# Kernel tuning notes

Measured on AMD Instinct MI355X. Metric: run time of the kernel, lower is better.

## Reference

```python
import jax, jax.numpy as jnp
import numpy as np

B, S, E, H = 2, 2048, 1024, 16
DH = E // H


def setup_inputs() -> dict:
    key = jax.random.key(0)
    ks = jax.random.split(key, 12)
    std = 1.0 / np.sqrt(E)
    inp = {
        "query": jax.random.normal(ks[0], (B, S, E), jnp.float32),
        "key": jax.random.normal(ks[1], (B, S, E), jnp.float32),
        "value": jax.random.normal(ks[2], (B, S, E), jnp.float32),
        "mask": jax.random.randint(ks[3], (B, 1, 1, S), 0, 2, jnp.int32),
        "Wq": jax.random.normal(ks[4], (E, E), jnp.float32) * std,
        "bq": jnp.zeros((E,), jnp.float32),
        "Wk": jax.random.normal(ks[5], (E, E), jnp.float32) * std,
        "bk": jnp.zeros((E,), jnp.float32),
        "Wv": jax.random.normal(ks[6], (E, E), jnp.float32) * std,
        "bv": jnp.zeros((E,), jnp.float32),
        "Wo": jax.random.normal(ks[7], (E, E), jnp.float32) * std,
        "bo": jnp.zeros((E,), jnp.float32),
    }
    return inp


def reference(query, key, value, mask, Wq, bq, Wk, bk, Wv, bv, Wo, bo):
    b = query.shape[0]
    # QKV projections, then split heads: [B,S,E] -> [B,H,S,Dh]
    def split_heads(x):
        return x.reshape(b, -1, H, DH).transpose(0, 2, 1, 3)
    q = split_heads(query @ Wq + bq)
    k = split_heads(key @ Wk + bk)
    v = split_heads(value @ Wv + bv)
    # explicit bmm -> mask -> softmax -> bmm (non-SDPA), scores [B,H,Sq,Sk]
    scores = jnp.einsum("bhqd,bhkd->bhqk", q, k) / np.sqrt(DH).astype(np.float32)
    scores = jnp.where(mask == 0, jnp.float32(-1e9), scores)
    attn = jax.nn.softmax(scores, axis=-1)  # dropout is identity in eval mode
    out = jnp.einsum("bhqk,bhkd->bhqd", attn, v)
    out = out.transpose(0, 2, 1, 3).reshape(b, -1, E)  # merge heads
    return out @ Wo + bo
```

## Files before the change

kernel.cpp:

```cpp
#include <hip/hip_runtime.h>
#include <hip/hip_bf16.h>
#include <stdint.h>

#define B_ 2
#define S_ 2048
#define E_ 1024
#define H_ 16
#define DH_ 64
#define MELEMS (4096 * 1024)
#define WE (1024 * 1024)

typedef unsigned short u16;
typedef __bf16 bf16x8 __attribute__((ext_vector_type(8)));
typedef u16 u16x8 __attribute__((ext_vector_type(8)));
typedef u16 u16x4 __attribute__((ext_vector_type(4)));
typedef float f32x4 __attribute__((ext_vector_type(4)));
typedef uint32_t u32x4 __attribute__((ext_vector_type(4)));
typedef uint32_t u32x2v __attribute__((ext_vector_type(2)));

__device__ __forceinline__ float bf2f(u16 u) {
    union { uint32_t i; float f; } v; v.i = ((uint32_t)u) << 16; return v.f;
}
__device__ __forceinline__ u16 f2bf(float f) {
    union { float f; uint32_t i; } v; v.f = f;
    uint32_t r = (v.i + 0x7FFFu + ((v.i >> 16) & 1u)) >> 16;
    return (u16)r;
}
__device__ __forceinline__ uint32_t pkbf(float a, float b) {
    __hip_bfloat162 h = __float22bfloat162_rn(make_float2(a, b));
    uint32_t r; __builtin_memcpy(&r, &h, 4);
    return r;
}
__device__ __forceinline__ bf16x8 ldfrag(const u16* p) {
    u16x8 t = *(const u16x8*)p;
    return __builtin_bit_cast(bf16x8, t);
}
__device__ __forceinline__ void gld16(const void* g, void* l) {
    __builtin_amdgcn_global_load_lds(
        (const __attribute__((address_space(1))) void*)g,
        (__attribute__((address_space(3))) void*)l, 16, 0, 0);
}

__global__ __launch_bounds__(256)
void cvt_all(const float* __restrict__ q, const float* __restrict__ k,
             const float* __restrict__ v,
             const float* __restrict__ W0, const float* __restrict__ W1,
             const float* __restrict__ W2, const float* __restrict__ W3,
             u16* __restrict__ Qi, u16* __restrict__ Ki, u16* __restrict__ Vi,
             u16* __restrict__ T0, u16* __restrict__ T1,
             u16* __restrict__ T2, u16* __restrict__ T3)
{
    __shared__ float tile[64][65];
    const int bid = blockIdx.x;
    const int tid = threadIdx.x;

    if (bid < 6144) {
        const int z = bid >> 11;
        const int cx = bid & 2047;
        const float* src = (z == 0) ? q : (z == 1) ? k : v;
        u16* dst = (z == 0) ? Qi : (z == 1) ? Ki : Vi;
        const size_t i8 = ((size_t)cx * 256 + tid) * 8;
        float4 f0 = *(const float4*)&src[i8];
        float4 f1 = *(const float4*)&src[i8 + 4];
        u16x8 t;
        t[0] = f2bf(f0.x); t[1] = f2bf(f0.y); t[2] = f2bf(f0.z); t[3] = f2bf(f0.w);
        t[4] = f2bf(f1.x); t[5] = f2bf(f1.y); t[6] = f2bf(f1.z); t[7] = f2bf(f1.w);
        *(u16x8*)&dst[i8] = t;
    } else {
        const int rr = bid - 6144;
        const int z = rr >> 8;
        const int tt = rr & 255;
        const float* W = (z == 0) ? W0 : (z == 1) ? W1 : (z == 2) ? W2 : W3;
        u16* T = (z == 0) ? T0 : (z == 1) ? T1 : (z == 2) ? T2 : T3;
        const int n0 = (tt & 15) * 64, k0 = (tt >> 4) * 64;
        const int r = tid >> 2, c0 = (tid & 3) * 16;

        #pragma unroll
        for (int i = 0; i < 4; ++i) {
            float4 w = *(const float4*)&W[(size_t)(k0 + r) * 1024 + n0 + c0 + i * 4];
            tile[r][c0 + i * 4 + 0] = w.x; tile[r][c0 + i * 4 + 1] = w.y;
            tile[r][c0 + i * 4 + 2] = w.z; tile[r][c0 + i * 4 + 3] = w.w;
        }
        __syncthreads();
        u16x8 a, b;
        #pragma unroll
        for (int j = 0; j < 8; ++j) a[j] = f2bf(tile[c0 + j][r]);
        #pragma unroll
        for (int j = 0; j < 8; ++j) b[j] = f2bf(tile[c0 + 8 + j][r]);
        *(u16x8*)&T[(size_t)(n0 + r) * 1024 + k0 + c0] = a;
        *(u16x8*)&T[(size_t)(n0 + r) * 1024 + k0 + c0 + 8] = b;
    }
}

template<int BN>
__global__ __launch_bounds__(256)
void gemm_bt(const u16* __restrict__ A0, const u16* __restrict__ A1,
             const u16* __restrict__ A2,
             const u16* __restrict__ Bt0, const u16* __restrict__ Bt1,
             const u16* __restrict__ Bt2,
             const float* __restrict__ b0, const float* __restrict__ b1,
             const float* __restrict__ b2,
             void* __restrict__ C0, void* __restrict__ C1, void* __restrict__ C2,
             const int* __restrict__ mask,
             int c_f32, int vt_z, float scale0, int K)
{
    const int z = blockIdx.z;
    const u16* A  = (z == 0) ? A0 : (z == 1) ? A1 : A2;
    const u16* Bt = (z == 0) ? Bt0 : (z == 1) ? Bt1 : Bt2;
    const float* bias = (z == 0) ? b0 : (z == 1) ? b1 : b2;
    void* C = (z == 0) ? C0 : (z == 1) ? C1 : C2;
    const float scale = (z == 0) ? scale0 : 1.0f;

    __shared__ alignas(16) u16 As[128 * 32];
    __shared__ alignas(16) u16 Bs[BN * 32];

    const int tid  = threadIdx.x;
    const int lane = tid & 63;
    const int wv   = tid >> 6;
    const int l15  = lane & 15;
    const int quad = lane >> 4;
    const int m0 = blockIdx.y * 128;
    const int n0 = blockIdx.x * BN;
    const int wr = (wv >> 1) * 64;
    const int wc = (wv & 1) * (BN / 2);

    const int srow = wv * 16 + (lane >> 2);
    const int skk  = (lane & 3) * 8;

    constexpr int NJ = BN / 32;
    f32x4 acc[4][NJ] = {};

    for (int k0 = 0; k0 < K; k0 += 32) {
        __syncthreads();
        #pragma unroll
        for (int h = 0; h < 2; ++h) {
            const int r = h * 64 + srow;
            gld16(&A[(size_t)(m0 + r) * K + k0 + skk], &As[r * 32 + skk]);
        }
        #pragma unroll
        for (int h = 0; h < BN / 64; ++h) {
            const int r = h * 64 + srow;
            gld16(&Bt[(size_t)(n0 + r) * K + k0 + skk], &Bs[r * 32 + skk]);
        }
        __syncthreads();

        bf16x8 a[4], b[NJ];
        #pragma unroll
        for (int i = 0; i < 4; ++i)
            a[i] = ldfrag(&As[(wr + i * 16 + l15) * 32 + quad * 8]);
        #pragma unroll
        for (int j = 0; j < NJ; ++j)
            b[j] = ldfrag(&Bs[(wc + j * 16 + l15) * 32 + quad * 8]);
        #pragma unroll
        for (int i = 0; i < 4; ++i)
            #pragma unroll
            for (int j = 0; j < NJ; ++j)
                acc[i][j] = __builtin_amdgcn_mfma_f32_16x16x32_bf16(
                    a[i], b[j], acc[i][j], 0, 0, 0);
    }

    #pragma unroll
    for (int j = 0; j < NJ; ++j) {
        const int col = n0 + wc + j * 16 + l15;
        const float bcol = bias[col];
        #pragma unroll
        for (int i = 0; i < 4; ++i) {
            if (z == vt_z) {
                const int row0 = m0 + wr + i * 16 + quad * 4;
                const int bb = row0 >> 11, s0 = row0 & 2047;
                const int4 mv = *(const int4*)&mask[bb * S_ + s0];
                u16x4 t;
                t[0] = mv.x ? f2bf((acc[i][j][0] + bcol) * scale) : (u16)0;
                t[1] = mv.y ? f2bf((acc[i][j][1] + bcol) * scale) : (u16)0;
                t[2] = mv.z ? f2bf((acc[i][j][2] + bcol) * scale) : (u16)0;
                t[3] = mv.w ? f2bf((acc[i][j][3] + bcol) * scale) : (u16)0;
                *(u16x4*)&((u16*)C)[((size_t)bb * E_ + col) * S_ + s0] = t;
            } else {
                #pragma unroll
                for (int r = 0; r < 4; ++r) {
                    const int row = m0 + wr + i * 16 + quad * 4 + r;
                    const float v = (acc[i][j][r] + bcol) * scale;
                    if (c_f32) ((float*)C)[(size_t)row * 1024 + col] = v;
                    else       ((u16*)C)[(size_t)row * 1024 + col]  = f2bf(v);
                }
            }
        }
    }
}

__global__ __launch_bounds__(512, 4)
void attn_v7(const u16* __restrict__ Q, const u16* __restrict__ K,
             const u16* __restrict__ Vt_g, const int* __restrict__ mask,
             u16* __restrict__ ctx)
{
    __shared__ alignas(16) u16 Ks[2][64 * 64];
    __shared__ alignas(16) u16 Vs[2][64 * 64];
    __shared__ alignas(16) u16 Mbf[S_];

    const int tid  = threadIdx.x;
    const int lane = tid & 63;
    const int wv   = tid >> 6;
    const int l15  = lane & 15;
    const int quad = lane >> 4;
    const int sw   = l15 & 7;
    const int kq   = (quad & 1) * 2 + (quad >> 1);
    const int qt = blockIdx.x;
    const int bh = blockIdx.y;
    const int b  = bh >> 4, h = bh & 15;

    const size_t qk_off = (size_t)b * S_ * E_ + (size_t)h * DH_;
    const size_t vt_off = ((size_t)b * E_ + (size_t)h * DH_) * S_;
    const int* mrow = &mask[b * S_];

    {
        const int i = tid * 4;
        const int4 m = *(const int4*)&mrow[i];
        u16x4 t;
        t[0] = m.x ? (u16)0x3F80 : (u16)0;
        t[1] = m.y ? (u16)0x3F80 : (u16)0;
        t[2] = m.z ? (u16)0x3F80 : (u16)0;
        t[3] = m.w ? (u16)0x3F80 : (u16)0;
        *(u16x4*)&Mbf[i] = t;
    }

    const int qr = qt * 128 + wv * 16 + l15;
    const bf16x8 qa0 = ldfrag(&Q[qk_off + (size_t)qr * E_ + quad * 8]);
    const bf16x8 qa1 = ldfrag(&Q[qk_off + (size_t)qr * E_ + 32 + quad * 8]);

    f32x4 oacc[4] = {};
    f32x4 lacc = {};

    const int kidx = tid & 255;
    const int grp  = tid >> 8;
    const int srow = kidx >> 3;
    const int sp   = kidx & 7;
    const int sg   = sp ^ (srow & 7);

    auto stage = [&](int kc, int buf) {
        #pragma unroll
        for (int g = 0; g < 2; ++g) {
            const int r = g * 32 + srow;
            if (grp == 0)
                gld16(&K[qk_off + (size_t)(kc + r) * E_ + sg * 8],
                      &Ks[buf][r * 64 + sp * 8]);
            else
                gld16(&Vt_g[vt_off + (size_t)r * S_ + kc + sg * 8],
                      &Vs[buf][r * 64 + sp * 8]);
        }
    };

    stage(0, 0);
    int cur = 0;

    for (int kc = 0; kc < S_; kc += 64) {
        __syncthreads();
        if (kc + 64 < S_) stage(kc + 64, cur ^ 1);

        bf16x8 pa[2];
        #pragma unroll
        for (int hh = 0; hh < 2; ++hh) {
            f32x4 st[2];
            #pragma unroll
            for (int tt = 0; tt < 2; ++tt) {
                const int R = (hh * 2 + tt) * 16 + l15;
                bf16x8 kf0 = ldfrag(&Ks[cur][R * 64 + (quad ^ sw) * 8]);
                bf16x8 kf1 = ldfrag(&Ks[cur][R * 64 + ((4 + quad) ^ sw) * 8]);
                f32x4 s = {};
                s = __builtin_amdgcn_mfma_f32_16x16x32_bf16(kf0, qa0, s, 0, 0, 0);
                s = __builtin_amdgcn_mfma_f32_16x16x32_bf16(kf1, qa1, s, 0, 0, 0);
                st[tt] = s;
            }
            const float e00 = __builtin_exp2f(st[0][0]);
            const float e01 = __builtin_exp2f(st[0][1]);
            const float e02 = __builtin_exp2f(st[0][2]);
            const float e03 = __builtin_exp2f(st[0][3]);
            const float e10 = __builtin_exp2f(st[1][0]);
            const float e11 = __builtin_exp2f(st[1][1]);
            const float e12 = __builtin_exp2f(st[1][2]);
            const float e13 = __builtin_exp2f(st[1][3]);
            const uint32_t wA = pkbf(e00, e01);
            const uint32_t wB = pkbf(e02, e03);
            const uint32_t wC = pkbf(e10, e11);
            const uint32_t wD = pkbf(e12, e13);
            u32x2v rAC = __builtin_amdgcn_permlane16_swap(wA, wC, false, false);
            u32x2v rBD = __builtin_amdgcn_permlane16_swap(wB, wD, false, false);
            u32x4 w;
            w[0] = rAC[0]; w[1] = rBD[0]; w[2] = rAC[1]; w[3] = rBD[1];
            pa[hh] = __builtin_bit_cast(bf16x8, w);
        }

        {
            bf16x8 mb0 = ldfrag(&Mbf[kc + kq * 8]);
            bf16x8 mb1 = ldfrag(&Mbf[kc + 32 + kq * 8]);
            lacc = __builtin_amdgcn_mfma_f32_16x16x32_bf16(pa[0], mb0, lacc, 0, 0, 0);
            lacc = __builtin_amdgcn_mfma_f32_16x16x32_bf16(pa[1], mb1, lacc, 0, 0, 0);
        }

        #pragma unroll
        for (int c = 0; c < 4; ++c) {
            const int Dd = c * 16 + l15;
            bf16x8 vb0 = ldfrag(&Vs[cur][Dd * 64 + ((0 + kq) ^ sw) * 8]);
            bf16x8 vb1 = ldfrag(&Vs[cur][Dd * 64 + ((4 + kq) ^ sw) * 8]);
            oacc[c] = __builtin_amdgcn_mfma_f32_16x16x32_bf16(pa[0], vb0, oacc[c], 0, 0, 0);
            oacc[c] = __builtin_amdgcn_mfma_f32_16x16x32_bf16(pa[1], vb1, oacc[c], 0, 0, 0);
        }
        cur ^= 1;
    }

    #pragma unroll
    for (int c = 0; c < 4; ++c) {
        const int e = h * DH_ + c * 16 + l15;
        #pragma unroll
        for (int r = 0; r < 4; ++r) {
            const int qg = qt * 128 + wv * 16 + quad * 4 + r;
            ctx[((size_t)b * S_ + qg) * E_ + e] = f2bf(oacc[c][r] / lacc[r]);
        }
    }
}

__global__ __launch_bounds__(256)
void gemm_bias(const void* __restrict__ A, int a_f32,
               const float* __restrict__ W, const float* __restrict__ bias,
               void* __restrict__ C, int c_f32,
               int M, int N, int K, float scale)
{
    __shared__ alignas(16) u16 As[64 * 32];
    __shared__ alignas(16) u16 Wt[64 * 32];
    const int tid  = threadIdx.x;
    const int lane = tid & 63;
    const int wv   = tid >> 6;
    const int l15  = lane & 15;
    const int quad = lane >> 4;
    const int m0 = blockIdx.y * 64, n0 = blockIdx.x * 64;
    const int wr = (wv >> 1) * 32, wc = (wv & 1) * 32;
    const int ar = tid >> 2, ac = (tid & 3) * 8;
    const int wk = tid >> 3, wn = (tid & 7) * 8;
    f32x4 acc[2][2] = {};
    for (int k0 = 0; k0 < K; k0 += 32) {
        __syncthreads();
        if (a_f32) {
            const float* Af = (const float*)A;
            const float* p = &Af[(size_t)(m0 + ar) * K + k0 + ac];
            float4 f0 = *(const float4*)p; float4 f1 = *(const float4*)(p + 4);
            u16x8 t;
            t[0] = f2bf(f0.x); t[1] = f2bf(f0.y); t[2] = f2bf(f0.z); t[3] = f2bf(f0.w);
            t[4] = f2bf(f1.x); t[5] = f2bf(f1.y); t[6] = f2bf(f1.z); t[7] = f2bf(f1.w);
            *(u16x8*)&As[ar * 32 + ac] = t;
        } else {
            const u16* Ab = (const u16*)A;
            *(u16x8*)&As[ar * 32 + ac] = *(const u16x8*)&Ab[(size_t)(m0 + ar) * K + k0 + ac];
        }
        {
            const float* p = &W[(size_t)(k0 + wk) * N + n0 + wn];
            float4 g0 = *(const float4*)p; float4 g1 = *(const float4*)(p + 4);
            float fv[8] = {g0.x, g0.y, g0.z, g0.w, g1.x, g1.y, g1.z, g1.w};
            #pragma unroll
            for (int j = 0; j < 8; ++j) Wt[(wn + j) * 32 + wk] = f2bf(fv[j]);
        }
        __syncthreads();
        bf16x8 a[2], b[2];
        #pragma unroll
        for (int sm = 0; sm < 2; ++sm) a[sm] = ldfrag(&As[(wr + sm * 16 + l15) * 32 + quad * 8]);
        #pragma unroll
        for (int sn = 0; sn < 2; ++sn) b[sn] = ldfrag(&Wt[(wc + sn * 16 + l15) * 32 + quad * 8]);
        #pragma unroll
        for (int sm = 0; sm < 2; ++sm)
            #pragma unroll
            for (int sn = 0; sn < 2; ++sn)
                acc[sm][sn] = __builtin_amdgcn_mfma_f32_16x16x32_bf16(a[sm], b[sn], acc[sm][sn], 0, 0, 0);
    }
    #pragma unroll
    for (int sm = 0; sm < 2; ++sm)
        #pragma unroll
        for (int sn = 0; sn < 2; ++sn) {
            const int col = n0 + wc + sn * 16 + l15;
            const float bcol = bias[col];
            #pragma unroll
            for (int r = 0; r < 4; ++r) {
                const int row = m0 + wr + sm * 16 + quad * 4 + r;
                const float v = (acc[sm][sn][r] + bcol) * scale;
                if (c_f32) ((float*)C)[(size_t)row * N + col] = v;
                else       ((u16*)C)[(size_t)row * N + col]  = f2bf(v);
            }
        }
}

__global__ __launch_bounds__(256)
void attn_v2(const u16* __restrict__ Q, const u16* __restrict__ K,
             const u16* __restrict__ V, const int* __restrict__ mask,
             u16* __restrict__ ctx, int BH_per_B)
{
    __shared__ alignas(16) u16 Ks[64 * 72];
    __shared__ alignas(16) u16 Vt[64 * 72];
    __shared__ alignas(16) u16 Pb[4][16 * 72];
    const int tid  = threadIdx.x;
    const int lane = tid & 63;
    const int wv   = tid >> 6;
    const int l15  = lane & 15;
    const int quad = lane >> 4;
    const int qt = blockIdx.x;
    const int bh = blockIdx.y;
    const int b  = bh / BH_per_B, h = bh % BH_per_B;
    const size_t headoff = (size_t)b * S_ * E_ + (size_t)h * DH_;
    const int qrow = qt * 64 + wv * 16 + l15;
    const bf16x8 qf0 = ldfrag(&Q[headoff + (size_t)qrow * E_ + quad * 8]);
    const bf16x8 qf1 = ldfrag(&Q[headoff + (size_t)qrow * E_ + 32 + quad * 8]);
    f32x4 oacc[4] = {};
    float mrun[4] = {-1e30f, -1e30f, -1e30f, -1e30f};
    float lrun[4] = {0.f, 0.f, 0.f, 0.f};
    const int skey = tid >> 2;
    const int sd0  = (tid & 3) * 16;
    for (int kc = 0; kc < S_; kc += 64) {
        __syncthreads();
        {
            const u16* kg = &K[headoff + (size_t)(kc + skey) * E_ + sd0];
            *(u16x8*)&Ks[skey * 72 + sd0]     = *(const u16x8*)kg;
            *(u16x8*)&Ks[skey * 72 + sd0 + 8] = *(const u16x8*)(kg + 8);
            const u16* vg = &V[headoff + (size_t)(kc + skey) * E_ + sd0];
            u16x8 v0 = *(const u16x8*)vg;
            u16x8 v1 = *(const u16x8*)(vg + 8);
            #pragma unroll
            for (int j = 0; j < 8; ++j) {
                const int d = sd0 + j;
                Vt[d * 72 + (skey ^ (((d >> 3) & 7) * 8))] = v0[j];
            }
            #pragma unroll
            for (int j = 0; j < 8; ++j) {
                const int d = sd0 + 8 + j;
                Vt[d * 72 + (skey ^ (((d >> 3) & 7) * 8))] = v1[j];
            }
        }
        __syncthreads();
        f32x4 sb[4];
        #pragma unroll
        for (int t = 0; t < 4; ++t) {
            bf16x8 kf0 = ldfrag(&Ks[(t * 16 + l15) * 72 + quad * 8]);
            bf16x8 kf1 = ldfrag(&Ks[(t * 16 + l15) * 72 + 32 + quad * 8]);
            f32x4 s = {};
            s = __builtin_amdgcn_mfma_f32_16x16x32_bf16(qf0, kf0, s, 0, 0, 0);
            s = __builtin_amdgcn_mfma_f32_16x16x32_bf16(qf1, kf1, s, 0, 0, 0);
            const int mv = mask[b * S_ + kc + t * 16 + l15];
            #pragma unroll
            for (int r = 0; r < 4; ++r) sb[t][r] = (mv == 0) ? -1e9f : s[r];
        }
        #pragma unroll
        for (int r = 0; r < 4; ++r) {
            float m = fmaxf(fmaxf(sb[0][r], sb[1][r]), fmaxf(sb[2][r], sb[3][r]));
            #pragma unroll
            for (int off = 1; off < 16; off <<= 1) m = fmaxf(m, __shfl_xor(m, off));
            const float mnew  = fmaxf(mrun[r], m);
            const float alpha = __expf(mrun[r] - mnew);
            mrun[r] = mnew;
            float sum = 0.f;
            #pragma unroll
            for (int t = 0; t < 4; ++t) {
                const float p = __expf(sb[t][r] - mnew);
                sb[t][r] = p; sum += p;
            }
            #pragma unroll
            for (int off = 1; off < 16; off <<= 1) sum += __shfl_xor(sum, off);
            lrun[r] = lrun[r] * alpha + sum;
            #pragma unroll
            for (int c = 0; c < 4; ++c) oacc[c][r] *= alpha;
        }
        #pragma unroll
        for (int t = 0; t < 4; ++t)
            #pragma unroll
            for (int r = 0; r < 4; ++r)
                Pb[wv][(quad * 4 + r) * 72 + t * 16 + l15] = f2bf(sb[t][r]);
        const bf16x8 pa0 = ldfrag(&Pb[wv][l15 * 72 + quad * 8]);
        const bf16x8 pa1 = ldfrag(&Pb[wv][l15 * 72 + 32 + quad * 8]);
        #pragma unroll
        for (int c = 0; c < 4; ++c) {
            const int d = c * 16 + l15;
            const int sg = ((d >> 3) & 7) * 8;
            bf16x8 vb0 = ldfrag(&Vt[d * 72 + ((quad * 8) ^ sg)]);
            bf16x8 vb1 = ldfrag(&Vt[d * 72 + ((32 + quad * 8) ^ sg)]);
            oacc[c] = __builtin_amdgcn_mfma_f32_16x16x32_bf16(pa0, vb0, oacc[c], 0, 0, 0);
            oacc[c] = __builtin_amdgcn_mfma_f32_16x16x32_bf16(pa1, vb1, oacc[c], 0, 0, 0);
        }
    }
    #pragma unroll
    for (int c = 0; c < 4; ++c) {
        const int e = h * DH_ + c * 16 + l15;
        #pragma unroll
        for (int r = 0; r < 4; ++r) {
            const int qg = qt * 64 + wv * 16 + quad * 4 + r;
            ctx[((size_t)b * S_ + qg) * E_ + e] = f2bf(oacc[c][r] / lrun[r]);
        }
    }
}

extern "C" void kernel_launch(void* const* d_in, const int* in_sizes, int n_in,
                              void* d_out, int out_size, void* d_ws, size_t ws_size,
                              hipStream_t stream)
{
    const float* query = (const float*)d_in[0];
    const float* key   = (const float*)d_in[1];
    const float* value = (const float*)d_in[2];
    const int*   mask  = (const int*)d_in[3];
    const float* Wq = (const float*)d_in[4];  const float* bq = (const float*)d_in[5];
    const float* Wk = (const float*)d_in[6];  const float* bk = (const float*)d_in[7];
    const float* Wv = (const float*)d_in[8];  const float* bv = (const float*)d_in[9];
    const float* Wo = (const float*)d_in[10]; const float* bo = (const float*)d_in[11];
    float* out = (float*)d_out;

    u16* ws = (u16*)d_ws;
    dim3 blk(256);

    const size_t need_fancy = (size_t)(6 * MELEMS + 4 * WE) * sizeof(u16);
    const size_t need_full  = (size_t)(4 * MELEMS) * sizeof(u16) + 64;

    if (ws_size >= need_fancy) {
        u16* Qi  = ws;
        u16* Ki  = Qi + MELEMS;
        u16* Vi  = Ki + MELEMS;
        u16* Wqt = Vi + MELEMS;
        u16* Wkt = Wqt + WE;
        u16* Wvt = Wkt + WE;
        u16* Wot = Wvt + WE;
        u16* Qp  = Wot + WE;
        u16* Kp  = Qp + MELEMS;
        u16* Vp  = Kp + MELEMS;
        u16* Cp  = Qi;

        cvt_all<<<dim3(7168), blk, 0, stream>>>(query, key, value,
                                                Wq, Wk, Wv, Wo,
                                                Qi, Ki, Vi, Wqt, Wkt, Wvt, Wot);

        gemm_bt<128><<<dim3(8, 32, 3), blk, 0, stream>>>(
            Qi, Ki, Vi, Wqt, Wkt, Wvt, bq, bk, bv,
            Qp, Kp, Vp, mask, 0, 2, 0.125f * 1.44269504f, E_);

        attn_v7<<<dim3(S_ / 128, B_ * H_), dim3(512), 0, stream>>>(
            Qp, Kp, Vp, mask, Cp);

        gemm_bt<64><<<dim3(16, 32, 1), blk, 0, stream>>>(
            Cp, Cp, Cp, Wot, Wot, Wot, bo, bo, bo,
            out, out, out, mask, 1, -1, 1.0f, E_);
    } else if (ws_size >= need_full) {
        u16* Qp = ws;
        u16* Kp = ws + MELEMS;
        u16* Vp = ws + 2 * MELEMS;
        u16* Cp = ws + 3 * MELEMS;
        const int M = B_ * S_;
        dim3 gg(E_ / 64, M / 64);
        gemm_bias<<<gg, blk, 0, stream>>>(query, 1, Wq, bq, Qp, 0, M, E_, E_, 0.125f);
        gemm_bias<<<gg, blk, 0, stream>>>(key,   1, Wk, bk, Kp, 0, M, E_, E_, 1.0f);
        gemm_bias<<<gg, blk, 0, stream>>>(value, 1, Wv, bv, Vp, 0, M, E_, E_, 1.0f);
        attn_v2<<<dim3(S_ / 64, B_ * H_), blk, 0, stream>>>(Qp, Kp, Vp, mask, Cp, H_);
        gemm_bias<<<gg, blk, 0, stream>>>(Cp, 0, Wo, bo, out, 1, M, E_, E_, 1.0f);
    } else {
        const size_t szb = (size_t)S_ * E_;
        u16* Qp = ws; u16* Kp = ws + szb; u16* Vp = ws + 2 * szb; u16* Cp = ws + 3 * szb;
        dim3 gg(E_ / 64, S_ / 64);
        for (int b = 0; b < B_; ++b) {
            gemm_bias<<<gg, blk, 0, stream>>>(query + b * szb, 1, Wq, bq, Qp, 0, S_, E_, E_, 0.125f);
            gemm_bias<<<gg, blk, 0, stream>>>(key   + b * szb, 1, Wk, bk, Kp, 0, S_, E_, E_, 1.0f);
            gemm_bias<<<gg, blk, 0, stream>>>(value + b * szb, 1, Wv, bv, Vp, 0, S_, E_, E_, 1.0f);
            attn_v2<<<dim3(S_ / 64, H_), blk, 0, stream>>>(Qp, Kp, Vp, mask + b * S_, Cp, H_);
            gemm_bias<<<gg, blk, 0, stream>>>(Cp, 0, Wo, bo, ((float*)d_out) + b * szb, 1, S_, E_, E_, 1.0f);
        }
    }
}
```

Before: 151.6 us.

## Restructure attention to 32x32 MFMA tiles with split-key waves and reduction

The attention kernel moves from 16x16x32 MFMA tiles to 32x32x16 tiles. Each wave now covers 32 queries, and the two wave groups each handle half of a 128-key chunk. Their partial outputs and row sums are combined through shared memory at the end. The aim is fewer LDS fragment loads per FLOP and half as many loop iterations and barriers, at the cost of larger accumulators, more register pressure and a final cross-wave reduction.

```diff
diff --git a/kernel.cpp b/kernel.cpp
--- a/kernel.cpp
+++ b/kernel.cpp
@@ -15,6 +15,7 @@
 typedef u16 u16x8 __attribute__((ext_vector_type(8)));
 typedef u16 u16x4 __attribute__((ext_vector_type(4)));
 typedef float f32x4 __attribute__((ext_vector_type(4)));
+typedef float f32x16 __attribute__((ext_vector_type(16)));
 typedef uint32_t u32x4 __attribute__((ext_vector_type(4)));
 typedef uint32_t u32x2v __attribute__((ext_vector_type(2)));
 
@@ -189,21 +190,22 @@
 }
 
 __global__ __launch_bounds__(512, 4)
-void attn_v7(const u16* __restrict__ Q, const u16* __restrict__ K,
+void attn_v8(const u16* __restrict__ Q, const u16* __restrict__ K,
              const u16* __restrict__ Vt_g, const int* __restrict__ mask,
              u16* __restrict__ ctx)
 {
-    __shared__ alignas(16) u16 Ks[2][64 * 64];
-    __shared__ alignas(16) u16 Vs[2][64 * 64];
+    __shared__ alignas(16) u16 smem[2][16384];
     __shared__ alignas(16) u16 Mbf[S_];
 
     const int tid  = threadIdx.x;
     const int lane = tid & 63;
     const int wv   = tid >> 6;
-    const int l15  = lane & 15;
-    const int quad = lane >> 4;
-    const int sw   = l15 & 7;
-    const int kq   = (quad & 1) * 2 + (quad >> 1);
+    const int l31  = lane & 31;
+    const int half = lane >> 5;
+    const int sw7  = lane & 7;
+    const int qw   = wv & 3;
+    const int kh   = wv >> 2;
+    const int kbase = kh * 64;
     const int qt = blockIdx.x;
     const int bh = blockIdx.y;
     const int b  = bh >> 4, h = bh & 15;
@@ -223,98 +225,116 @@
         *(u16x4*)&Mbf[i] = t;
     }
 
-    const int qr = qt * 128 + wv * 16 + l15;
-    const bf16x8 qa0 = ldfrag(&Q[qk_off + (size_t)qr * E_ + quad * 8]);
-    const bf16x8 qa1 = ldfrag(&Q[qk_off + (size_t)qr * E_ + 32 + quad * 8]);
-
-    f32x4 oacc[4] = {};
-    f32x4 lacc = {};
-
-    const int kidx = tid & 255;
-    const int grp  = tid >> 8;
-    const int srow = kidx >> 3;
-    const int sp   = kidx & 7;
-    const int sg   = sp ^ (srow & 7);
+    const int q0 = qt * 128 + qw * 32;
+    bf16x8 qf[4];
+    #pragma unroll
+    for (int s = 0; s < 4; ++s)
+        qf[s] = ldfrag(&Q[qk_off + (size_t)(q0 + l31) * E_ + s * 16 + half * 8]);
+
+    f32x16 O[2] = {};
+    f32x16 La  = {};
 
     auto stage = [&](int kc, int buf) {
+        u16* Kb = &smem[buf][0];
+        u16* Vb = &smem[buf][8192];
         #pragma unroll
         for (int g = 0; g < 2; ++g) {
-            const int r = g * 32 + srow;
-            if (grp == 0)
-                gld16(&K[qk_off + (size_t)(kc + r) * E_ + sg * 8],
-                      &Ks[buf][r * 64 + sp * 8]);
-            else
-                gld16(&Vt_g[vt_off + (size_t)r * S_ + kc + sg * 8],
-                      &Vs[buf][r * 64 + sp * 8]);
+            const int key = g * 64 + (tid >> 3);
+            const int ks  = tid & 7;
+            const int kd  = ks ^ (key & 7);
+            gld16(&K[qk_off + (size_t)(kc + key) * E_ + kd * 8],
+                  &Kb[key * 64 + ks * 8]);
+        }
+        #pragma unroll
+        for (int g = 0; g < 2; ++g) {
+            const int d  = g * 32 + (tid >> 4);
+            const int vs = tid & 15;
+            const int kb = (vs & 8) | ((vs & 7) ^ (d & 7));
+            gld16(&Vt_g[vt_off + (size_t)d * S_ + kc + kb * 8],
+                  &Vb[d * 128 + vs * 8]);
         }
     };
 
     stage(0, 0);
     int cur = 0;
 
-    for (int kc = 0; kc < S_; kc += 64) {
-        __syncthreads();
-        if (kc + 64 < S_) stage(kc + 64, cur ^ 1);
-
-        bf16x8 pa[2];
-        #pragma unroll
-        for (int hh = 0; hh < 2; ++hh) {
-            f32x4 st[2];
-            #pragma unroll
-            for (int tt = 0; tt < 2; ++tt) {
-                const int R = (hh * 2 + tt) * 16 + l15;
-                bf16x8 kf0 = ldfrag(&Ks[cur][R * 64 + (quad ^ sw) * 8]);
-                bf16x8 kf1 = ldfrag(&Ks[cur][R * 64 + ((4 + quad) ^ sw) * 8]);
-                f32x4 s = {};
-                s = __builtin_amdgcn_mfma_f32_16x16x32_bf16(kf0, qa0, s, 0, 0, 0);
-                s = __builtin_amdgcn_mfma_f32_16x16x32_bf16(kf1, qa1, s, 0, 0, 0);
-                st[tt] = s;
-            }
-            const float e00 = __builtin_exp2f(st[0][0]);
-            const float e01 = __builtin_exp2f(st[0][1]);
-            const float e02 = __builtin_exp2f(st[0][2]);
-            const float e03 = __builtin_exp2f(st[0][3]);
-            const float e10 = __builtin_exp2f(st[1][0]);
-            const float e11 = __builtin_exp2f(st[1][1]);
-            const float e12 = __builtin_exp2f(st[1][2]);
-            const float e13 = __builtin_exp2f(st[1][3]);
-            const uint32_t wA = pkbf(e00, e01);
-            const uint32_t wB = pkbf(e02, e03);
-            const uint32_t wC = pkbf(e10, e11);
-            const uint32_t wD = pkbf(e12, e13);
-            u32x2v rAC = __builtin_amdgcn_permlane16_swap(wA, wC, false, false);
-            u32x2v rBD = __builtin_amdgcn_permlane16_swap(wB, wD, false, false);
-            u32x4 w;
-            w[0] = rAC[0]; w[1] = rBD[0]; w[2] = rAC[1]; w[3] = rBD[1];
-            pa[hh] = __builtin_bit_cast(bf16x8, w);
-        }
-
-        {
-            bf16x8 mb0 = ldfrag(&Mbf[kc + kq * 8]);
-            bf16x8 mb1 = ldfrag(&Mbf[kc + 32 + kq * 8]);
-            lacc = __builtin_amdgcn_mfma_f32_16x16x32_bf16(pa[0], mb0, lacc, 0, 0, 0);
-            lacc = __builtin_amdgcn_mfma_f32_16x16x32_bf16(pa[1], mb1, lacc, 0, 0, 0);
-        }
-
-        #pragma unroll
-        for (int c = 0; c < 4; ++c) {
-            const int Dd = c * 16 + l15;
-            bf16x8 vb0 = ldfrag(&Vs[cur][Dd * 64 + ((0 + kq) ^ sw) * 8]);
-            bf16x8 vb1 = ldfrag(&Vs[cur][Dd * 64 + ((4 + kq) ^ sw) * 8]);
-            oacc[c] = __builtin_amdgcn_mfma_f32_16x16x32_bf16(pa[0], vb0, oacc[c], 0, 0, 0);
-            oacc[c] = __builtin_amdgcn_mfma_f32_16x16x32_bf16(pa[1], vb1, oacc[c], 0, 0, 0);
+    for (int kc = 0; kc < S_; kc += 128) {
+        __syncthreads();
+        if (kc + 128 < S_) stage(kc + 128, cur ^ 1);
+        const u16* Kb = &smem[cur][0];
+        const u16* Vb = &smem[cur][8192];
+
+        #pragma unroll
+        for (int kt = 0; kt < 2; ++kt) {
+            f32x16 St = {};
+            #pragma unroll
+            for (int s = 0; s < 4; ++s) {
+                bf16x8 kf = ldfrag(&Kb[(kbase + kt * 32 + l31) * 64 +
+                                       ((s * 2 + half) ^ sw7) * 8]);
+                St = __builtin_amdgcn_mfma_f32_32x32x16_bf16(kf, qf[s], St, 0, 0, 0);
+            }
+            float ex[16];
+            #pragma unroll
+            for (int i = 0; i < 16; ++i) ex[i] = __builtin_exp2f(St[i]);
+            const uint32_t w0 = pkbf(ex[0], ex[1]),  w1 = pkbf(ex[2], ex[3]);
+            const uint32_t w2 = pkbf(ex[4], ex[5]),  w3 = pkbf(ex[6], ex[7]);
+            const uint32_t w4 = pkbf(ex[8], ex[9]),  w5 = pkbf(ex[10], ex[11]);
+            const uint32_t w6 = pkbf(ex[12], ex[13]), w7 = pkbf(ex[14], ex[15]);
+            u32x2v r02 = __builtin_amdgcn_permlane32_swap(w0, w2, false, false);
+            u32x2v r13 = __builtin_amdgcn_permlane32_swap(w1, w3, false, false);
+            u32x2v r46 = __builtin_amdgcn_permlane32_swap(w4, w6, false, false);
+            u32x2v r57 = __builtin_amdgcn_permlane32_swap(w5, w7, false, false);
+            u32x4 f0, f1;
+            f0[0] = r02[0]; f0[1] = r13[0]; f0[2] = r02[1]; f0[3] = r13[1];
+            f1[0] = r46[0]; f1[1] = r57[0]; f1[2] = r46[1]; f1[3] = r57[1];
+            const bf16x8 pa0 = __builtin_bit_cast(bf16x8, f0);
+            const bf16x8 pa1 = __builtin_bit_cast(bf16x8, f1);
+
+            {
+                bf16x8 mb0 = ldfrag(&Mbf[kc + kbase + kt * 32 + half * 8]);
+                bf16x8 mb1 = ldfrag(&Mbf[kc + kbase + kt * 32 + 16 + half * 8]);
+                La = __builtin_amdgcn_mfma_f32_32x32x16_bf16(pa0, mb0, La, 0, 0, 0);
+                La = __builtin_amdgcn_mfma_f32_32x32x16_bf16(pa1, mb1, La, 0, 0, 0);
+            }
+            #pragma unroll
+            for (int nt = 0; nt < 2; ++nt) {
+                const int drow = nt * 32 + l31;
+                const int kb0 = kh * 8 + kt * 4 + half;
+                const int kb1 = kh * 8 + kt * 4 + 2 + half;
+                bf16x8 vb0 = ldfrag(&Vb[drow * 128 +
+                                        ((kb0 & 8) | ((kb0 & 7) ^ sw7)) * 8]);
+                bf16x8 vb1 = ldfrag(&Vb[drow * 128 +
+                                        ((kb1 & 8) | ((kb1 & 7) ^ sw7)) * 8]);
+                O[nt] = __builtin_amdgcn_mfma_f32_32x32x16_bf16(pa0, vb0, O[nt], 0, 0, 0);
+                O[nt] = __builtin_amdgcn_mfma_f32_32x32x16_bf16(pa1, vb1, O[nt], 0, 0, 0);
+            }
         }
         cur ^= 1;
     }
 
-    #pragma unroll
-    for (int c = 0; c < 4; ++c) {
-        const int e = h * DH_ + c * 16 + l15;
-        #pragma unroll
-        for (int r = 0; r < 4; ++r) {
-            const int qg = qt * 128 + wv * 16 + quad * 4 + r;
-            ctx[((size_t)b * S_ + qg) * E_ + e] = f2bf(oacc[c][r] / lacc[r]);
-        }
+    __syncthreads();
+    float* scr = (float*)smem;
+    const int sbase = (qw * 64 + lane) * 49;
+    if (kh == 1) {
+        #pragma unroll
+        for (int i = 0; i < 16; ++i) scr[sbase + i]      = O[0][i];
+        #pragma unroll
+        for (int i = 0; i < 16; ++i) scr[sbase + 16 + i] = O[1][i];
+        #pragma unroll
+        for (int i = 0; i < 16; ++i) scr[sbase + 32 + i] = La[i];
+    }
+    __syncthreads();
+    if (kh == 0) {
+        #pragma unroll
+        for (int nt = 0; nt < 2; ++nt)
+            #pragma unroll
+            for (int i = 0; i < 16; ++i) {
+                const float o = O[nt][i] + scr[sbase + nt * 16 + i];
+                const float l = La[i]    + scr[sbase + 32 + i];
+                const int q = q0 + (i & 3) + 8 * (i >> 2) + 4 * half;
+                const int e = h * DH_ + nt * 32 + l31;
+                ctx[((size_t)b * S_ + q) * E_ + e] = f2bf(o / l);
+            }
     }
 }
 
@@ -532,7 +552,7 @@
             Qi, Ki, Vi, Wqt, Wkt, Wvt, bq, bk, bv,
             Qp, Kp, Vp, mask, 0, 2, 0.125f * 1.44269504f, E_);
 
-        attn_v7<<<dim3(S_ / 128, B_ * H_), dim3(512), 0, stream>>>(
+        attn_v8<<<dim3(S_ / 128, B_ * H_), dim3(512), 0, stream>>>(
             Qp, Kp, Vp, mask, Cp);
 
         gemm_bt<64><<<dim3(16, 32, 1), blk, 0, stream>>>(
```

Result: no change. 154.0 us (+1.5%).
